# Optimization experiments

Hardware: AMD Instinct MI355X
Metric: run time of the kernel (lower is better)

The kernel has to match this reference:

```python
import jax, jax.numpy as jnp
import numpy as np

N, E, H, D, IN = 50000, 800000, 4, 16, 64  # nodes, edges, heads, head dim, in_feats
HD = H * D


def setup_inputs() -> dict:
    key = jax.random.key(0)
    ks = jax.random.split(key, 12)
    inp = {
        "q_src": jax.random.normal(ks[0], (N, H, D), jnp.float32),
        "v_src": jax.random.normal(ks[1], (N, H, D), jnp.float32),
        "feat": jax.random.normal(ks[2], (N, IN), jnp.float32),
        "src": jax.random.randint(ks[3], (E,), 0, N, jnp.int32),
        "dst": jax.random.randint(ks[4], (E,), 0, N, jnp.int32),
        # parameters (torch nn.Linear stores W as [out, in]; we use [in, out])
        "Wk": jax.random.normal(ks[5], (IN, HD), jnp.float32) / np.sqrt(IN),
        "bk": jnp.zeros((HD,), jnp.float32),
        "Wskip": jax.random.normal(ks[6], (IN, HD), jnp.float32) / np.sqrt(IN),
        "bskip": jnp.zeros((HD,), jnp.float32),
        "Wgate": jax.random.normal(ks[7], (3 * HD, 1), jnp.float32) / np.sqrt(3 * HD),
        "bgate": jnp.zeros((1,), jnp.float32),
        "ln_gamma": jnp.ones((HD,), jnp.float32),
        "ln_beta": jnp.zeros((HD,), jnp.float32),
        "prelu_a": jnp.array(0.25, jnp.float32),  # nn.PReLU() default
    }
    return inp


def reference(q_src, v_src, feat, src, dst, Wk, bk, Wskip, bskip, Wgate, bgate, ln_gamma, ln_beta, prelu_a):
    n = feat.shape[0]
    # k_dst = lin_key(h_dst).view(-1, H, D)
    k_dst = (feat @ Wk + bk).reshape(n, H, D)
    # per-edge dot-product scores: u_dot_v('ft','ft') -> [E, H, 1], scaled
    a = jnp.sum(q_src[src] * k_dst[dst], axis=-1, keepdims=True) / np.sqrt(D)
    # edge softmax over incoming edges of each dst node (segment softmax)
    amax = jax.lax.stop_gradient(jax.ops.segment_max(a, dst, num_segments=n))  # [n,H,1]
    ex = jnp.exp(a - amax[dst])
    denom = jax.ops.segment_sum(ex, dst, num_segments=n)  # [n,H,1]
    sa = ex / denom[dst]  # [E,H,1]
    # u_mul_e + sum: weighted scatter-sum aggregation
    agg = jax.ops.segment_sum(v_src[src] * sa, dst, num_segments=n)  # [n,H,D]
    rst = agg.reshape(n, HD)
    # skip connection + gate
    skip = feat @ Wskip + bskip  # [n, HD]
    gate = jax.nn.sigmoid(jnp.concatenate([skip, rst, skip - rst], axis=-1) @ Wgate + bgate)
    rst = gate * skip + (1.0 - gate) * rst
    # LayerNorm over last dim (eps=1e-5)
    mu = jnp.mean(rst, axis=-1, keepdims=True)
    var = jnp.mean(jnp.square(rst - mu), axis=-1, keepdims=True)
    rst = (rst - mu) * jax.lax.rsqrt(var + 1e-5) * ln_gamma + ln_beta
    # PReLU activation
    rst = jnp.where(rst >= 0, rst, prelu_a * rst)
    return rst
```

## Files before the change

kernel.cpp:

```cpp
#include <hip/hip_runtime.h>
#include <hip/hip_fp16.h>

#define NN 50000
#define EE 800000
#define MAXDEG 64
#define NBUCK 98
#define BSHIFT 9
#define BMASK 511
#define CAP 9216
#define AB_BLOCKS 1564

typedef _Float16 f16x8 __attribute__((ext_vector_type(8)));
typedef float    f32x4 __attribute__((ext_vector_type(4)));

union F4H { float4 f4; __half2 h2[4]; };

__global__ void zero_kernel(int* __restrict__ gcursor)
{
    if (threadIdx.x < NBUCK) gcursor[threadIdx.x] = 0;
}

__global__ __launch_bounds__(256) void binpack_kernel(
    const float* __restrict__ feat,
    const float* __restrict__ Wk, const float* __restrict__ bk,
    const float* __restrict__ Ws, const float* __restrict__ bs,
    const float* __restrict__ q, const float* __restrict__ v,
    const int* __restrict__ src, const int* __restrict__ dst,
    float* __restrict__ kdst, float* __restrict__ skip,
    __half2* __restrict__ qv, int* __restrict__ gcursor,
    int* __restrict__ staging)
{
    __shared__ f16x8 sFrag[16 * 64];
    __shared__ int hist[NBUCK], gbase[NBUCK];

    int tid = threadIdx.x, bid = blockIdx.x;

    if ((bid & 1) == 0) {
        if (tid < NBUCK) hist[tid] = 0;
        __syncthreads();

        int ebid  = bid >> 1;
        int ebase = ebid * 1024 + tid * 4;
        int4 es, ed;
        int b0 = 0, b1 = 0, b2 = 0, b3 = 0, r0 = 0, r1 = 0, r2 = 0, r3 = 0;
        bool ev = ebase < EE;
        if (ev) {
            es = *(const int4*)(src + ebase);
            ed = *(const int4*)(dst + ebase);
            b0 = ed.x >> BSHIFT; r0 = atomicAdd(&hist[b0], 1);
            b1 = ed.y >> BSHIFT; r1 = atomicAdd(&hist[b1], 1);
            b2 = ed.z >> BSHIFT; r2 = atomicAdd(&hist[b2], 1);
            b3 = ed.w >> BSHIFT; r3 = atomicAdd(&hist[b3], 1);
        }
        __syncthreads();
        if (tid < NBUCK) {
            int h = hist[tid];
            gbase[tid] = h ? atomicAdd(gcursor + tid, h) : 0;
        }
        __syncthreads();
        if (ev) {
            int i0 = gbase[b0] + r0; if (i0 < CAP) staging[b0 * CAP + i0] = (es.x << BSHIFT) | (ed.x & BMASK);
            int i1 = gbase[b1] + r1; if (i1 < CAP) staging[b1 * CAP + i1] = (es.y << BSHIFT) | (ed.y & BMASK);
            int i2 = gbase[b2] + r2; if (i2 < CAP) staging[b2 * CAP + i2] = (es.z << BSHIFT) | (ed.z & BMASK);
            int i3 = gbase[b3] + r3; if (i3 < CAP) staging[b3 * CAP + i3] = (es.w << BSHIFT) | (ed.w & BMASK);
        }
        return;
    }

    int nbid = bid >> 1;
    int wave = tid >> 6, lane = tid & 63;

    for (int i = tid; i < 4096; i += 256) {
        int k = i >> 6, nk = i & 63;
        int kt = k >> 5, j = k & 7;
        int lf = ((k >> 3) & 3) * 16 + (nk & 15);
        ((_Float16*)&sFrag[((nk >> 4) * 2 + kt) * 64 + lf])[j]       = (_Float16)Wk[i];
        ((_Float16*)&sFrag[((4 + (nk >> 4)) * 2 + kt) * 64 + lf])[j] = (_Float16)Ws[i];
    }
    __syncthreads();

    int base16 = nbid * 64 + wave * 16;
    if (base16 < NN) {
        int m  = lane & 15;
        int kg = lane >> 4;
        const float* arow = feat + (size_t)(base16 + m) * 64 + kg * 8;
        float4 fa0 = *(const float4*)(arow + 0);
        float4 fa1 = *(const float4*)(arow + 4);
        float4 fa2 = *(const float4*)(arow + 32);
        float4 fa3 = *(const float4*)(arow + 36);
        f16x8 a0 = { (_Float16)fa0.x,(_Float16)fa0.y,(_Float16)fa0.z,(_Float16)fa0.w,
                     (_Float16)fa1.x,(_Float16)fa1.y,(_Float16)fa1.z,(_Float16)fa1.w };
        f16x8 a1 = { (_Float16)fa2.x,(_Float16)fa2.y,(_Float16)fa2.z,(_Float16)fa2.w,
                     (_Float16)fa3.x,(_Float16)fa3.y,(_Float16)fa3.z,(_Float16)fa3.w };

        f32x4 acc0={0,0,0,0}, acc1={0,0,0,0}, acc2={0,0,0,0}, acc3={0,0,0,0};
        f32x4 acc4={0,0,0,0}, acc5={0,0,0,0}, acc6={0,0,0,0}, acc7={0,0,0,0};

#define COLT(c, ACC) { \
        f16x8 b0 = sFrag[((c)*2 + 0) * 64 + lane]; \
        f16x8 b1 = sFrag[((c)*2 + 1) * 64 + lane]; \
        ACC = __builtin_amdgcn_mfma_f32_16x16x32_f16(a0, b0, ACC, 0, 0, 0); \
        ACC = __builtin_amdgcn_mfma_f32_16x16x32_f16(a1, b1, ACC, 0, 0, 0); }
        COLT(0, acc0) COLT(1, acc1) COLT(2, acc2) COLT(3, acc3)
        COLT(4, acc4) COLT(5, acc5) COLT(6, acc6) COLT(7, acc7)
#undef COLT

        int rbase = base16 + kg * 4;

#define STOREC(P, COFF, BIAS, ACC) { \
        int col = (COFF) + m; float bb = BIAS[col]; \
        P[(size_t)(rbase + 0) * 64 + col] = ACC[0] + bb; \
        P[(size_t)(rbase + 1) * 64 + col] = ACC[1] + bb; \
        P[(size_t)(rbase + 2) * 64 + col] = ACC[2] + bb; \
        P[(size_t)(rbase + 3) * 64 + col] = ACC[3] + bb; }
        STOREC(kdst,  0, bk, acc0) STOREC(kdst, 16, bk, acc1)
        STOREC(kdst, 32, bk, acc2) STOREC(kdst, 48, bk, acc3)
        STOREC(skip,  0, bs, acc4) STOREC(skip, 16, bs, acc5)
        STOREC(skip, 32, bs, acc6) STOREC(skip, 48, bs, acc7)
#undef STOREC
    }

    {
        size_t g0 = (size_t)nbid * 4096 + (size_t)tid * 16;
        if ((int)(g0 >> 6) < NN) {
            const float4* qp = (const float4*)(q + g0);
            const float4* vp = (const float4*)(v + g0);
            #pragma unroll
            for (int gI = 0; gI < 4; ++gI) {
                float4 qq = qp[gI], vv = vp[gI];
                F4H outw;
                outw.h2[0] = __floats2half2_rn(qq.x, vv.x);
                outw.h2[1] = __floats2half2_rn(qq.y, vv.y);
                outw.h2[2] = __floats2half2_rn(qq.z, vv.z);
                outw.h2[3] = __floats2half2_rn(qq.w, vv.w);
                *(float4*)(qv + g0 + gI * 4) = outw.f4;
            }
        }
    }
}

__global__ __launch_bounds__(256) void scatter_kernel(
    const int* __restrict__ staging, const int* __restrict__ gcursor,
    unsigned short* __restrict__ sorted_src,
    int* __restrict__ cntA, int* __restrict__ cntB)
{
    __shared__ int cnt[512];
    int b = blockIdx.x >> 1, half = blockIdx.x & 1, tid = threadIdx.x;
    cnt[tid] = 0; cnt[tid + 256] = 0;
    __syncthreads();

    int nE = gcursor[b];
    if (nE > CAP) nE = CAP;
    int lo = half ? (nE >> 1) : 0;
    int hi = half ? nE : (nE >> 1);

    if (half == 0) {
        for (int i = lo + tid; i < hi; i += 256) {
            int e  = staging[b * CAP + i];
            int dl = e & BMASK;
            int pos = atomicAdd(&cnt[dl], 1);
            if (pos < MAXDEG)
                sorted_src[(size_t)((b << BSHIFT) + dl) * MAXDEG + pos] =
                    (unsigned short)(e >> BSHIFT);
        }
    } else {
        for (int i = lo + tid; i < hi; i += 256) {
            int e  = staging[b * CAP + i];
            int dl = e & BMASK;
            int pos = atomicAdd(&cnt[dl], 1);
            int sl = MAXDEG - 1 - pos;
            if (sl >= 0)
                sorted_src[(size_t)((b << BSHIFT) + dl) * MAXDEG + sl] =
                    (unsigned short)(e >> BSHIFT);
        }
    }
    __syncthreads();

    int* cp = half ? cntB : cntA;
    int d0 = (b << BSHIFT) + tid;
    if (d0 < NN) cp[d0] = cnt[tid];
    int d1 = d0 + 256;
    if (d1 < NN) cp[d1] = cnt[tid + 256];
}

__global__ __launch_bounds__(256) void gather_finalize_kernel(
    const __half2* __restrict__ qv,
    const float*   __restrict__ kdst,
    const float*   __restrict__ skipb,
    const unsigned short* __restrict__ sorted_src,
    const int*     __restrict__ cntA,
    const int*     __restrict__ cntB,
    const float*   __restrict__ Wg,
    const float*   __restrict__ bg,
    const float*   __restrict__ gamma,
    const float*   __restrict__ beta,
    const float*   __restrict__ prelu_a,
    float* __restrict__ out, int n)
{
    int node = (blockIdx.x * 256 + threadIdx.x) >> 6;
    int lane = threadIdx.x & 63;
    if (node >= n) return;
    int g = lane >> 4;
    int w = lane & 15;
    int slot = w * 4;

    int cA = cntA[node];
    int cB = cntB[node];
    int dcount = cA + cB;
    if (dcount > MAXDEG) dcount = MAXDEG;
    int sidx = (lane < cA) ? lane : (MAXDEG - 1 - (lane - cA));
    int s_all = (lane < dcount) ? (int)sorted_src[(size_t)node * MAXDEG + sidx] : 0;

    float4 k4  = *(const float4*)(kdst  + (size_t)node * 64 + slot);
    float4 sk4 = *(const float4*)(skipb + (size_t)node * 64 + slot);
    float wg0a = Wg[slot],      wg1a = Wg[slot+1],      wg2a = Wg[slot+2],      wg3a = Wg[slot+3];
    float wg0b = Wg[64+slot],   wg1b = Wg[64+slot+1],   wg2b = Wg[64+slot+2],   wg3b = Wg[64+slot+3];
    float wg0c = Wg[128+slot],  wg1c = Wg[128+slot+1],  wg2c = Wg[128+slot+2],  wg3c = Wg[128+slot+3];
    float gm0 = gamma[slot], gm1 = gamma[slot+1], gm2 = gamma[slot+2], gm3 = gamma[slot+3];
    float bt0 = beta[slot],  bt1 = beta[slot+1],  bt2 = beta[slot+2],  bt3 = beta[slot+3];
    float bgv = bg[0];
    float al  = prelu_a[0];

    float den = 0.f;
    float acc0 = 0.f, acc1 = 0.f, acc2 = 0.f, acc3 = 0.f;

    int niter = (dcount + 15) >> 4;
    if (niter > 0) {
        F4H rA, rB, rC, rD;
        rA.f4 = *(const float4*)(qv + (size_t)__shfl(s_all,  g)      * 64 + slot);
        rB.f4 = *(const float4*)(qv + (size_t)__shfl(s_all,  4 + g)  * 64 + slot);
        rC.f4 = *(const float4*)(qv + (size_t)__shfl(s_all,  8 + g)  * 64 + slot);
        rD.f4 = *(const float4*)(qv + (size_t)__shfl(s_all, 12 + g)  * 64 + slot);

        for (int it = 0; it < niter; ++it) {
            F4H cAx = rA, cBx = rB, cCx = rC, cDx = rD;
            int e0 = it * 16 + g;
            if (it + 1 < niter) {
                rA.f4 = *(const float4*)(qv + (size_t)__shfl(s_all, (e0 + 16) & 63) * 64 + slot);
                rB.f4 = *(const float4*)(qv + (size_t)__shfl(s_all, (e0 + 20) & 63) * 64 + slot);
                rC.f4 = *(const float4*)(qv + (size_t)__shfl(s_all, (e0 + 24) & 63) * 64 + slot);
                rD.f4 = *(const float4*)(qv + (size_t)__shfl(s_all, (e0 + 28) & 63) * 64 + slot);
            }

#define STREAM(CX, EOFF) { \
            float2 a0 = __half22float2(CX.h2[0]); \
            float2 a1 = __half22float2(CX.h2[1]); \
            float2 a2 = __half22float2(CX.h2[2]); \
            float2 a3 = __half22float2(CX.h2[3]); \
            float p = a0.x * k4.x + a1.x * k4.y + a2.x * k4.z + a3.x * k4.w; \
            p += __shfl_xor(p, 1); \
            p += __shfl_xor(p, 2); \
            float ex = ((e0 + (EOFF)) < dcount) ? __expf(p * 0.25f) : 0.f; \
            den += ex; \
            acc0 = fmaf(ex, a0.y, acc0); \
            acc1 = fmaf(ex, a1.y, acc1); \
            acc2 = fmaf(ex, a2.y, acc2); \
            acc3 = fmaf(ex, a3.y, acc3); }

            STREAM(cAx, 0)
            STREAM(cBx, 4)
            STREAM(cCx, 8)
            STREAM(cDx, 12)
#undef STREAM
        }
    }

    den  += __shfl_xor(den, 16);  den  += __shfl_xor(den, 32);
    acc0 += __shfl_xor(acc0, 16); acc0 += __shfl_xor(acc0, 32);
    acc1 += __shfl_xor(acc1, 16); acc1 += __shfl_xor(acc1, 32);
    acc2 += __shfl_xor(acc2, 16); acc2 += __shfl_xor(acc2, 32);
    acc3 += __shfl_xor(acc3, 16); acc3 += __shfl_xor(acc3, 32);

    float inv = (den > 0.f) ? 1.f / den : 0.f;
    float r0 = acc0 * inv, r1 = acc1 * inv, r2 = acc2 * inv, r3 = acc3 * inv;

    float gp = sk4.x * wg0a + r0 * wg0b + (sk4.x - r0) * wg0c
             + sk4.y * wg1a + r1 * wg1b + (sk4.y - r1) * wg1c
             + sk4.z * wg2a + r2 * wg2b + (sk4.z - r2) * wg2c
             + sk4.w * wg3a + r3 * wg3b + (sk4.w - r3) * wg3c;
    gp += __shfl_xor(gp, 1);
    gp += __shfl_xor(gp, 2);
    gp += __shfl_xor(gp, 4);
    gp += __shfl_xor(gp, 8);
    float gate = 1.f / (1.f + __expf(-(gp + bgv)));

    float m0 = gate * sk4.x + (1.f - gate) * r0;
    float m1 = gate * sk4.y + (1.f - gate) * r1;
    float m2 = gate * sk4.z + (1.f - gate) * r2;
    float m3 = gate * sk4.w + (1.f - gate) * r3;

    float mu = m0 + m1 + m2 + m3;
    mu += __shfl_xor(mu, 1); mu += __shfl_xor(mu, 2);
    mu += __shfl_xor(mu, 4); mu += __shfl_xor(mu, 8);
    mu *= (1.f / 64.f);
    float d0 = m0 - mu, d1 = m1 - mu, d2 = m2 - mu, d3 = m3 - mu;
    float var = d0 * d0 + d1 * d1 + d2 * d2 + d3 * d3;
    var += __shfl_xor(var, 1); var += __shfl_xor(var, 2);
    var += __shfl_xor(var, 4); var += __shfl_xor(var, 8);
    var *= (1.f / 64.f);
    float rs = rsqrtf(var + 1e-5f);

    float y0 = d0 * rs * gm0 + bt0;
    float y1 = d1 * rs * gm1 + bt1;
    float y2 = d2 * rs * gm2 + bt2;
    float y3 = d3 * rs * gm3 + bt3;
    y0 = (y0 >= 0.f) ? y0 : al * y0;
    y1 = (y1 >= 0.f) ? y1 : al * y1;
    y2 = (y2 >= 0.f) ? y2 : al * y2;
    y3 = (y3 >= 0.f) ? y3 : al * y3;

    if (g == 0) {
        float4 o; o.x = y0; o.y = y1; o.z = y2; o.w = y3;
        *(float4*)(out + (size_t)node * 64 + slot) = o;
    }
}

extern "C" void kernel_launch(void* const* d_in, const int* in_sizes, int n_in,
                              void* d_out, int out_size, void* d_ws, size_t ws_size,
                              hipStream_t stream)
{
    const float* q_src  = (const float*)d_in[0];
    const float* v_src  = (const float*)d_in[1];
    const float* feat   = (const float*)d_in[2];
    const int*   src    = (const int*)d_in[3];
    const int*   dst    = (const int*)d_in[4];
    const float* Wk     = (const float*)d_in[5];
    const float* bk     = (const float*)d_in[6];
    const float* Wskip  = (const float*)d_in[7];
    const float* bskip  = (const float*)d_in[8];
    const float* Wgate  = (const float*)d_in[9];
    const float* bgate  = (const float*)d_in[10];
    const float* ln_g   = (const float*)d_in[11];
    const float* ln_b   = (const float*)d_in[12];
    const float* prelu  = (const float*)d_in[13];

    float* out = (float*)d_out;

    char* ws = (char*)d_ws;
    const size_t A = (size_t)NN * 64 * 4;
    float*          kdst       = (float*)(ws);
    float*          skip       = (float*)(ws + A);
    __half2*        qv         = (__half2*)(ws + 2 * A);
    unsigned short* sorted_src = (unsigned short*)(ws + 3 * A);
    size_t off = 3 * A + A / 2;
    int* cntA    = (int*)(ws + off);            off += (size_t)NN * 4;
    int* cntB    = (int*)(ws + off);            off += (size_t)NN * 4;
    int* gcursor = (int*)(ws + off);            off += 4096;
    int* staging = (int*)(ws + off);

    zero_kernel<<<1, 128, 0, stream>>>(gcursor);

    binpack_kernel<<<AB_BLOCKS, 256, 0, stream>>>(
        feat, Wk, bk, Wskip, bskip, q_src, v_src, src, dst,
        kdst, skip, qv, gcursor, staging);

    scatter_kernel<<<NBUCK * 2, 256, 0, stream>>>(staging, gcursor,
                                                  sorted_src, cntA, cntB);

    int gblk = (NN * 64 + 255) / 256;
    gather_finalize_kernel<<<gblk, 256, 0, stream>>>(qv, kdst, skip,
                                                     sorted_src, cntA, cntB,
                                                     Wgate, bgate, ln_g, ln_b,
                                                     prelu, out, NN);
}
```

Measured before the change: 88.84 us.

## Pack k_dst and skip into interleaved fp16 buffer; shrink gather batch to 8 edges

The GEMM epilogue now writes k_dst and skip as interleaved half2 pairs into one buffer instead of two fp32 arrays. This halves the bytes written by binpack and read by the gather kernel. The gather loop also processes 8 edges per iteration instead of 16 and skips the second half-batch when it is past the degree, so low-degree nodes waste less work. The cost is fp16 rounding of k and skip, plus less memory-level parallelism from having fewer loads in flight per iteration.

```diff
diff --git a/kernel.cpp b/kernel.cpp
--- a/kernel.cpp
+++ b/kernel.cpp
@@ -26,7 +26,7 @@
     const float* __restrict__ Ws, const float* __restrict__ bs,
     const float* __restrict__ q, const float* __restrict__ v,
     const int* __restrict__ src, const int* __restrict__ dst,
-    float* __restrict__ kdst, float* __restrict__ skip,
+    __half2* __restrict__ ks,
     __half2* __restrict__ qv, int* __restrict__ gcursor,
     int* __restrict__ staging)
 {
@@ -107,17 +107,15 @@
 
         int rbase = base16 + kg * 4;
 
-#define STOREC(P, COFF, BIAS, ACC) { \
-        int col = (COFF) + m; float bb = BIAS[col]; \
-        P[(size_t)(rbase + 0) * 64 + col] = ACC[0] + bb; \
-        P[(size_t)(rbase + 1) * 64 + col] = ACC[1] + bb; \
-        P[(size_t)(rbase + 2) * 64 + col] = ACC[2] + bb; \
-        P[(size_t)(rbase + 3) * 64 + col] = ACC[3] + bb; }
-        STOREC(kdst,  0, bk, acc0) STOREC(kdst, 16, bk, acc1)
-        STOREC(kdst, 32, bk, acc2) STOREC(kdst, 48, bk, acc3)
-        STOREC(skip,  0, bs, acc4) STOREC(skip, 16, bs, acc5)
-        STOREC(skip, 32, bs, acc6) STOREC(skip, 48, bs, acc7)
-#undef STOREC
+#define STOREP(COFF, AK, AS) { \
+        int col = (COFF) + m; float bbk = bk[col], bbs = bs[col]; \
+        ks[(size_t)(rbase + 0) * 64 + col] = __floats2half2_rn(AK[0] + bbk, AS[0] + bbs); \
+        ks[(size_t)(rbase + 1) * 64 + col] = __floats2half2_rn(AK[1] + bbk, AS[1] + bbs); \
+        ks[(size_t)(rbase + 2) * 64 + col] = __floats2half2_rn(AK[2] + bbk, AS[2] + bbs); \
+        ks[(size_t)(rbase + 3) * 64 + col] = __floats2half2_rn(AK[3] + bbk, AS[3] + bbs); }
+        STOREP( 0, acc0, acc4) STOREP(16, acc1, acc5)
+        STOREP(32, acc2, acc6) STOREP(48, acc3, acc7)
+#undef STOREP
     }
 
     {
@@ -185,8 +183,7 @@
 
 __global__ __launch_bounds__(256) void gather_finalize_kernel(
     const __half2* __restrict__ qv,
-    const float*   __restrict__ kdst,
-    const float*   __restrict__ skipb,
+    const __half2* __restrict__ ks,
     const unsigned short* __restrict__ sorted_src,
     const int*     __restrict__ cntA,
     const int*     __restrict__ cntB,
@@ -205,14 +202,20 @@
     int slot = w * 4;
 
     int cA = cntA[node];
-    int cB = cntB[node];
-    int dcount = cA + cB;
+    int dcount = cA + cntB[node];
     if (dcount > MAXDEG) dcount = MAXDEG;
     int sidx = (lane < cA) ? lane : (MAXDEG - 1 - (lane - cA));
     int s_all = (lane < dcount) ? (int)sorted_src[(size_t)node * MAXDEG + sidx] : 0;
 
-    float4 k4  = *(const float4*)(kdst  + (size_t)node * 64 + slot);
-    float4 sk4 = *(const float4*)(skipb + (size_t)node * 64 + slot);
+    F4H ksr;
+    ksr.f4 = *(const float4*)(ks + (size_t)node * 64 + slot);
+    float2 ks0 = __half22float2(ksr.h2[0]);
+    float2 ks1 = __half22float2(ksr.h2[1]);
+    float2 ks2 = __half22float2(ksr.h2[2]);
+    float2 ks3 = __half22float2(ksr.h2[3]);
+    float4 k4;  k4.x = ks0.x;  k4.y = ks1.x;  k4.z = ks2.x;  k4.w = ks3.x;
+    float4 sk4; sk4.x = ks0.y; sk4.y = ks1.y; sk4.z = ks2.y; sk4.w = ks3.y;
+
     float wg0a = Wg[slot],      wg1a = Wg[slot+1],      wg2a = Wg[slot+2],      wg3a = Wg[slot+3];
     float wg0b = Wg[64+slot],   wg1b = Wg[64+slot+1],   wg2b = Wg[64+slot+2],   wg3b = Wg[64+slot+3];
     float wg0c = Wg[128+slot],  wg1c = Wg[128+slot+1],  wg2c = Wg[128+slot+2],  wg3c = Wg[128+slot+3];
@@ -224,44 +227,55 @@
     float den = 0.f;
     float acc0 = 0.f, acc1 = 0.f, acc2 = 0.f, acc3 = 0.f;
 
-    int niter = (dcount + 15) >> 4;
+    int niter = (dcount + 7) >> 3;
     if (niter > 0) {
-        F4H rA, rB, rC, rD;
-        rA.f4 = *(const float4*)(qv + (size_t)__shfl(s_all,  g)      * 64 + slot);
-        rB.f4 = *(const float4*)(qv + (size_t)__shfl(s_all,  4 + g)  * 64 + slot);
-        rC.f4 = *(const float4*)(qv + (size_t)__shfl(s_all,  8 + g)  * 64 + slot);
-        rD.f4 = *(const float4*)(qv + (size_t)__shfl(s_all, 12 + g)  * 64 + slot);
+        int sA = __shfl(s_all, g);
+        int sB = __shfl(s_all, 4 + g);
+        F4H rA, rB;
+        rA.f4 = *(const float4*)(qv + (size_t)sA * 64 + slot);
+        rB.f4 = *(const float4*)(qv + (size_t)sB * 64 + slot);
 
         for (int it = 0; it < niter; ++it) {
-            F4H cAx = rA, cBx = rB, cCx = rC, cDx = rD;
-            int e0 = it * 16 + g;
+            F4H cAx = rA, cBx = rB;
+            int e0 = it * 8;
             if (it + 1 < niter) {
-                rA.f4 = *(const float4*)(qv + (size_t)__shfl(s_all, (e0 + 16) & 63) * 64 + slot);
-                rB.f4 = *(const float4*)(qv + (size_t)__shfl(s_all, (e0 + 20) & 63) * 64 + slot);
-                rC.f4 = *(const float4*)(qv + (size_t)__shfl(s_all, (e0 + 24) & 63) * 64 + slot);
-                rD.f4 = *(const float4*)(qv + (size_t)__shfl(s_all, (e0 + 28) & 63) * 64 + slot);
+                int sA2 = __shfl(s_all, (e0 + 8 + g) & 63);
+                int sB2 = __shfl(s_all, (e0 + 12 + g) & 63);
+                rA.f4 = *(const float4*)(qv + (size_t)sA2 * 64 + slot);
+                rB.f4 = *(const float4*)(qv + (size_t)sB2 * 64 + slot);
             }
 
-#define STREAM(CX, EOFF) { \
-            float2 a0 = __half22float2(CX.h2[0]); \
-            float2 a1 = __half22float2(CX.h2[1]); \
-            float2 a2 = __half22float2(CX.h2[2]); \
-            float2 a3 = __half22float2(CX.h2[3]); \
-            float p = a0.x * k4.x + a1.x * k4.y + a2.x * k4.z + a3.x * k4.w; \
-            p += __shfl_xor(p, 1); \
-            p += __shfl_xor(p, 2); \
-            float ex = ((e0 + (EOFF)) < dcount) ? __expf(p * 0.25f) : 0.f; \
-            den += ex; \
-            acc0 = fmaf(ex, a0.y, acc0); \
-            acc1 = fmaf(ex, a1.y, acc1); \
-            acc2 = fmaf(ex, a2.y, acc2); \
-            acc3 = fmaf(ex, a3.y, acc3); }
-
-            STREAM(cAx, 0)
-            STREAM(cBx, 4)
-            STREAM(cCx, 8)
-            STREAM(cDx, 12)
-#undef STREAM
+            {
+                float2 a0 = __half22float2(cAx.h2[0]);
+                float2 a1 = __half22float2(cAx.h2[1]);
+                float2 a2 = __half22float2(cAx.h2[2]);
+                float2 a3 = __half22float2(cAx.h2[3]);
+                float p = a0.x * k4.x + a1.x * k4.y + a2.x * k4.z + a3.x * k4.w;
+                p += __shfl_xor(p, 1);
+                p += __shfl_xor(p, 2);
+                float ex = ((e0 + g) < dcount) ? __expf(p * 0.25f) : 0.f;
+                den += ex;
+                acc0 = fmaf(ex, a0.y, acc0);
+                acc1 = fmaf(ex, a1.y, acc1);
+                acc2 = fmaf(ex, a2.y, acc2);
+                acc3 = fmaf(ex, a3.y, acc3);
+            }
+
+            if (e0 + 4 < dcount) {
+                float2 b0 = __half22float2(cBx.h2[0]);
+                float2 b1 = __half22float2(cBx.h2[1]);
+                float2 b2 = __half22float2(cBx.h2[2]);
+                float2 b3 = __half22float2(cBx.h2[3]);
+                float p = b0.x * k4.x + b1.x * k4.y + b2.x * k4.z + b3.x * k4.w;
+                p += __shfl_xor(p, 1);
+                p += __shfl_xor(p, 2);
+                float ex = ((e0 + 4 + g) < dcount) ? __expf(p * 0.25f) : 0.f;
+                den += ex;
+                acc0 = fmaf(ex, b0.y, acc0);
+                acc1 = fmaf(ex, b1.y, acc1);
+                acc2 = fmaf(ex, b2.y, acc2);
+                acc3 = fmaf(ex, b3.y, acc3);
+            }
         }
     }
 
@@ -338,11 +352,10 @@
 
     char* ws = (char*)d_ws;
     const size_t A = (size_t)NN * 64 * 4;
-    float*          kdst       = (float*)(ws);
-    float*          skip       = (float*)(ws + A);
-    __half2*        qv         = (__half2*)(ws + 2 * A);
-    unsigned short* sorted_src = (unsigned short*)(ws + 3 * A);
-    size_t off = 3 * A + A / 2;
+    __half2*        ks         = (__half2*)(ws);
+    __half2*        qv         = (__half2*)(ws + A);
+    unsigned short* sorted_src = (unsigned short*)(ws + 2 * A);
+    size_t off = 2 * A + A / 2;
     int* cntA    = (int*)(ws + off);            off += (size_t)NN * 4;
     int* cntB    = (int*)(ws + off);            off += (size_t)NN * 4;
     int* gcursor = (int*)(ws + off);            off += 4096;
@@ -352,13 +365,13 @@
 
     binpack_kernel<<<AB_BLOCKS, 256, 0, stream>>>(
         feat, Wk, bk, Wskip, bskip, q_src, v_src, src, dst,
-        kdst, skip, qv, gcursor, staging);
+        ks, qv, gcursor, staging);
 
     scatter_kernel<<<NBUCK * 2, 256, 0, stream>>>(staging, gcursor,
                                                   sorted_src, cntA, cntB);
 
     int gblk = (NN * 64 + 255) / 256;
-    gather_finalize_kernel<<<gblk, 256, 0, stream>>>(qv, kdst, skip,
+    gather_finalize_kernel<<<gblk, 256, 0, stream>>>(qv, ks,
                                                      sorted_src, cntA, cntB,
                                                      Wgate, bgate, ln_g, ln_b,
                                                      prelu, out, NN);
```

After: 79.27 us. 10.8% less time.
